# Kernel optimization log

Hardware: AMD Instinct MI355X
Metric: run time of the kernel (lower is better)

The kernel has to match this reference:

```python
import jax, jax.numpy as jnp
import numpy as np

N = 30000      # total nodes across batch
E = 480000     # edges (before self-loops)
B = 48         # graphs in batch
H = 4          # heads
D = 64         # hidden per head
NIN = 8
NOUT = 128
L = 10
SLOPE = 0.2    # GATConv default negative_slope


def setup_inputs() -> dict:
    key = jax.random.key(0)
    ks = jax.random.split(key, 12)
    s = 0.05
    x = jax.random.normal(ks[0], (N, NIN), jnp.float32)
    edge_index = jax.random.randint(ks[1], (2, E), 0, N, dtype=jnp.int32)
    batch = jnp.sort(jax.random.randint(ks[2], (N,), 0, B, dtype=jnp.int32))
    # layer 0 params (input dim NIN)
    W0 = jax.random.normal(ks[3], (NIN, H * D), jnp.float32) * s
    a_src0 = jax.random.normal(ks[4], (H, D), jnp.float32) * s
    a_dst0 = jax.random.normal(ks[5], (H, D), jnp.float32) * s
    b0 = jnp.zeros((H * D,), jnp.float32)
    # layers 1..L-1 (input dim H*D)
    Ws = jax.random.normal(ks[6], (L - 1, H * D, H * D), jnp.float32) * s
    a_srcs = jax.random.normal(ks[7], (L - 1, H, D), jnp.float32) * s
    a_dsts = jax.random.normal(ks[8], (L - 1, H, D), jnp.float32) * s
    bs = jnp.zeros((L - 1, H * D), jnp.float32)
    # readout head: GELU -> Linear(4*H*D -> NOUT)
    head_W = jax.random.normal(ks[9], (4 * H * D, NOUT), jnp.float32) * s
    head_b = jnp.zeros((NOUT,), jnp.float32)
    return dict(x=x, edge_index=edge_index, batch=batch,
                W0=W0, a_src0=a_src0, a_dst0=a_dst0, b0=b0,
                Ws=Ws, a_srcs=a_srcs, a_dsts=a_dsts, bs=bs,
                head_W=head_W, head_b=head_b)


def _gat_layer(x, W, a_src, a_dst, b, src, dst):
    n = x.shape[0]
    h = (x @ W).reshape(n, H, D)                      # [N,H,D]
    alpha_src = jnp.einsum('nhd,hd->nh', h, a_src)    # [N,H]
    alpha_dst = jnp.einsum('nhd,hd->nh', h, a_dst)
    e = jax.nn.leaky_relu(alpha_src[src] + alpha_dst[dst], SLOPE)  # [Etot,H]
    # segment softmax over destination neighborhoods
    m = jax.ops.segment_max(e, dst, num_segments=n)
    e = jnp.exp(e - m[dst])
    z = jax.ops.segment_sum(e, dst, num_segments=n)
    alpha = e / (z[dst] + 1e-16)                      # [Etot,H]
    msg = h[src] * alpha[:, :, None]                  # [Etot,H,D]
    out = jax.ops.segment_sum(msg, dst, num_segments=n)
    return out.reshape(n, H * D) + b


def reference(x, edge_index, batch, W0, a_src0, a_dst0, b0,
              Ws, a_srcs, a_dsts, bs, head_W, head_b):
    # add self loops (GATConv default add_self_loops=True)
    loops = jnp.arange(N, dtype=edge_index.dtype)
    src = jnp.concatenate([edge_index[0], loops])
    dst = jnp.concatenate([edge_index[1], loops])

    h = _gat_layer(x, W0, a_src0, a_dst0, b0, src, dst)
    for i in range(L - 1):
        h = jax.nn.gelu(h, approximate=False)  # dropout = identity (eval)
        h = _gat_layer(h, Ws[i], a_srcs[i], a_dsts[i], bs[i], src, dst)

    # MultiAggregation([min, max, mean, sum]) over graphs
    cnt = jax.ops.segment_sum(jnp.ones((N,), h.dtype), batch, num_segments=B)
    g_sum = jax.ops.segment_sum(h, batch, num_segments=B)
    g_mean = g_sum / jnp.maximum(cnt, 1.0)[:, None]
    g_min = jax.ops.segment_min(h, batch, num_segments=B)
    g_max = jax.ops.segment_max(h, batch, num_segments=B)
    g = jnp.concatenate([g_min, g_max, g_mean, g_sum], axis=-1)  # [B, 4*H*D]

    return jax.nn.gelu(g, approximate=False) @ head_W + head_b   # [B, NOUT]
```

## Files before the change

### kernel.cpp

```cpp
#include <hip/hip_runtime.h>
#include <math.h>

#define NN   30000
#define EE   480000
#define ETOT 510000
#define BB   48
#define HHH  4
#define DDD  64
#define CCH  256
#define NINP 8
#define NOUTP 128
#define NLAY 10
#define SLOPE 0.2f
#define PCHUNK 32

typedef short v8s  __attribute__((ext_vector_type(8)));
typedef float v4f  __attribute__((ext_vector_type(4)));

__device__ __forceinline__ float gelu_f(float x){
    return 0.5f * x * (1.0f + erff(x * 0.70710678118654752f));
}
__device__ __forceinline__ unsigned short f2bf(float f){
    unsigned u = __float_as_uint(f);
    unsigned r = u + 0x7FFF + ((u >> 16) & 1);
    return (unsigned short)(r >> 16);
}
__device__ __forceinline__ float bf2f(unsigned short b){
    return __uint_as_float(((unsigned)b) << 16);
}
__device__ __forceinline__ float lrelu(float e){
    return (e > 0.f) ? e : SLOPE * e;
}
__device__ __forceinline__ float4 up4(uint2 u){
    float4 r;
    r.x = __uint_as_float(u.x << 16);
    r.y = __uint_as_float(u.x & 0xFFFF0000u);
    r.z = __uint_as_float(u.y << 16);
    r.w = __uint_as_float(u.y & 0xFFFF0000u);
    return r;
}

__global__ void count_k(const int* __restrict__ ei, int* __restrict__ cnt){
    int e = blockIdx.x * 256 + threadIdx.x;
    if (e >= ETOT) return;
    int d = (e < EE) ? ei[EE + e] : (e - EE);
    atomicAdd(&cnt[d], 1);
}

__global__ __launch_bounds__(1024) void scan_k(const int* __restrict__ cnt, int* __restrict__ row_ptr){
    __shared__ int sdata[1024];
    __shared__ int carry;
    int tid = threadIdx.x;
    if (tid == 0) carry = 0;
    __syncthreads();
    for (int base = 0; base < NN; base += 1024){
        int i = base + tid;
        int v = (i < NN) ? cnt[i] : 0;
        sdata[tid] = v;
        __syncthreads();
        for (int off = 1; off < 1024; off <<= 1){
            int t = (tid >= off) ? sdata[tid - off] : 0;
            __syncthreads();
            sdata[tid] += t;
            __syncthreads();
        }
        if (i < NN) row_ptr[i] = carry + sdata[tid] - v;
        __syncthreads();
        if (tid == 1023) carry += sdata[1023];
        __syncthreads();
    }
    if (tid == 0) row_ptr[NN] = carry;
}

__global__ void scatter_k(const int* __restrict__ ei, const int* __restrict__ row_ptr,
                          int* __restrict__ cursor, int* __restrict__ csr_src){
    int e = blockIdx.x * 256 + threadIdx.x;
    if (e >= ETOT) return;
    int s, d;
    if (e < EE){ s = ei[e]; d = ei[EE + e]; } else { s = d = e - EE; }
    int pos = row_ptr[d] + atomicAdd(&cursor[d], 1);
    csr_src[pos] = s;
}

__global__ __launch_bounds__(256) void wconv_k(const float* __restrict__ Ws,
                                               unsigned short* __restrict__ WT_hi,
                                               unsigned short* __restrict__ WT_lo){
    int l = blockIdx.x;
    int n = threadIdx.x;
    int k0 = blockIdx.y * 32;
    const float* W = Ws + (size_t)l * CCH * CCH;
    unsigned short* th = WT_hi + (size_t)l * CCH * CCH;
    unsigned short* tl = WT_lo + (size_t)l * CCH * CCH;
    for (int k = k0; k < k0 + 32; ++k){
        float w = W[k * CCH + n];
        unsigned short h = f2bf(w);
        th[n * CCH + k] = h;
        tl[n * CCH + k] = f2bf(w - bf2f(h));
    }
}

__global__ __launch_bounds__(256) void waconv_k(const float* __restrict__ Ws,
                                                const float* __restrict__ a_srcs,
                                                const float* __restrict__ a_dsts,
                                                unsigned short* __restrict__ wa_hi,
                                                unsigned short* __restrict__ wa_lo){
    int l = blockIdx.x;
    int k = threadIdx.x;
    const float* W = Ws + (size_t)l * CCH * CCH;
#pragma unroll
    for (int j = 0; j < 8; ++j){
        const float* av = (j < 4) ? (a_srcs + (size_t)l * CCH + j * DDD)
                                  : (a_dsts + (size_t)l * CCH + (j - 4) * DDD);
        int cb = (j & 3) * DDD;
        float s = 0.f;
        for (int d = 0; d < DDD; ++d) s += W[k * CCH + cb + d] * av[d];
        unsigned short hb = f2bf(s);
        wa_hi[((size_t)l * 16 + j) * CCH + k] = hb;
        wa_lo[((size_t)l * 16 + j) * CCH + k] = f2bf(s - bf2f(hb));
    }
#pragma unroll
    for (int j = 8; j < 16; ++j){
        wa_hi[((size_t)l * 16 + j) * CCH + k] = 0;
        wa_lo[((size_t)l * 16 + j) * CCH + k] = 0;
    }
}

__global__ __launch_bounds__(256) void l0_fused(const float* __restrict__ x,
                                                const float* __restrict__ W0,
                                                const float* __restrict__ a_src,
                                                const float* __restrict__ a_dst,
                                                unsigned short* __restrict__ hout,
                                                float* __restrict__ asb,
                                                float* __restrict__ adb){
    __shared__ float xs[NINP];
    int n = blockIdx.x;
    int c = threadIdx.x;
    if (c < NINP) xs[c] = x[n * NINP + c];
    __syncthreads();
    float acc = 0.f;
#pragma unroll
    for (int k = 0; k < NINP; ++k) acc += xs[k] * W0[k * CCH + c];
    hout[(size_t)n * CCH + c] = f2bf(acc);
    int hh = c >> 6, lane = c & 63;
    float s1 = acc * a_src[hh * DDD + lane];
    float s2 = acc * a_dst[hh * DDD + lane];
#pragma unroll
    for (int off = 32; off; off >>= 1){
        s1 += __shfl_xor(s1, off);
        s2 += __shfl_xor(s2, off);
    }
    if (lane == 0){
        asb[(size_t)n * HHH + hh] = s1;
        adb[(size_t)n * HHH + hh] = s2;
    }
}

__global__ __launch_bounds__(256) void gemm_mfma(const float* __restrict__ A,
                                                 const unsigned short* __restrict__ Bhi,
                                                 const unsigned short* __restrict__ Blo,
                                                 const unsigned short* __restrict__ WAhi,
                                                 const unsigned short* __restrict__ WAlo,
                                                 unsigned short* __restrict__ C,
                                                 float* __restrict__ asb,
                                                 float* __restrict__ adb){
    int tid  = threadIdx.x;
    int lane = tid & 63, wave = tid >> 6;
    int wr = wave >> 1, wc = wave & 1;
    int rowBase = blockIdx.y * 128 + wr * 64;
    int colBase = blockIdx.x * 128 + wc * 64;
    int fr = lane & 15;
    int kg = lane >> 4;
    bool doAlpha = (blockIdx.x == 0) && (wc == 0);

    v4f acc[4][4];
#pragma unroll
    for (int mi = 0; mi < 4; ++mi)
#pragma unroll
        for (int ni = 0; ni < 4; ++ni) acc[mi][ni] = (v4f){0.f, 0.f, 0.f, 0.f};
    v4f acca[4];
#pragma unroll
    for (int mi = 0; mi < 4; ++mi) acca[mi] = (v4f){0.f, 0.f, 0.f, 0.f};

    const float* aptr[4];
#pragma unroll
    for (int mi = 0; mi < 4; ++mi){
        int r = rowBase + mi * 16 + fr;
        if (r >= NN) r = NN - 1;
        aptr[mi] = A + (size_t)r * CCH + kg * 8;
    }
    const unsigned short* bhp[4];
    const unsigned short* blp[4];
#pragma unroll
    for (int ni = 0; ni < 4; ++ni){
        int c = colBase + ni * 16 + fr;
        bhp[ni] = Bhi + (size_t)c * CCH + kg * 8;
        blp[ni] = Blo + (size_t)c * CCH + kg * 8;
    }
    const unsigned short* wahp = WAhi + (size_t)fr * CCH + kg * 8;
    const unsigned short* walp = WAlo + (size_t)fr * CCH + kg * 8;

    for (int kc = 0; kc < CCH; kc += 32){
        v8s ah[4], al[4], bh[4], bl[4];
#pragma unroll
        for (int mi = 0; mi < 4; ++mi){
            float4 v0 = *(const float4*)(aptr[mi] + kc);
            float4 v1 = *(const float4*)(aptr[mi] + kc + 4);
            float f[8] = {v0.x, v0.y, v0.z, v0.w, v1.x, v1.y, v1.z, v1.w};
            v8s hi, lo;
#pragma unroll
            for (int j = 0; j < 8; ++j){
                float g = gelu_f(f[j]);
                unsigned short hb = f2bf(g);
                hi[j] = (short)hb;
                lo[j] = (short)f2bf(g - bf2f(hb));
            }
            ah[mi] = hi; al[mi] = lo;
        }
#pragma unroll
        for (int ni = 0; ni < 4; ++ni){
            bh[ni] = *(const v8s*)(bhp[ni] + kc);
            bl[ni] = *(const v8s*)(blp[ni] + kc);
        }
#pragma unroll
        for (int mi = 0; mi < 4; ++mi)
#pragma unroll
            for (int ni = 0; ni < 4; ++ni){
                acc[mi][ni] = __builtin_amdgcn_mfma_f32_16x16x32_bf16(ah[mi], bh[ni], acc[mi][ni], 0, 0, 0);
                acc[mi][ni] = __builtin_amdgcn_mfma_f32_16x16x32_bf16(al[mi], bh[ni], acc[mi][ni], 0, 0, 0);
                acc[mi][ni] = __builtin_amdgcn_mfma_f32_16x16x32_bf16(ah[mi], bl[ni], acc[mi][ni], 0, 0, 0);
            }
        if (doAlpha){
            v8s wh = *(const v8s*)(wahp + kc);
            v8s wl = *(const v8s*)(walp + kc);
#pragma unroll
            for (int mi = 0; mi < 4; ++mi){
                acca[mi] = __builtin_amdgcn_mfma_f32_16x16x32_bf16(ah[mi], wh, acca[mi], 0, 0, 0);
                acca[mi] = __builtin_amdgcn_mfma_f32_16x16x32_bf16(al[mi], wh, acca[mi], 0, 0, 0);
                acca[mi] = __builtin_amdgcn_mfma_f32_16x16x32_bf16(ah[mi], wl, acca[mi], 0, 0, 0);
            }
        }
    }

#pragma unroll
    for (int mi = 0; mi < 4; ++mi)
#pragma unroll
        for (int j = 0; j < 4; ++j){
            int r = rowBase + mi * 16 + kg * 4 + j;
            if (r < NN){
#pragma unroll
                for (int ni = 0; ni < 4; ++ni)
                    C[(size_t)r * CCH + colBase + ni * 16 + fr] = f2bf(acc[mi][ni][j]);
            }
        }
    if (doAlpha){
#pragma unroll
        for (int mi = 0; mi < 4; ++mi)
#pragma unroll
            for (int j = 0; j < 4; ++j){
                int r = rowBase + mi * 16 + kg * 4 + j;
                if (r < NN){
                    float val = acca[mi][j];
                    if (fr < 4)      asb[(size_t)r * HHH + fr]       = val;
                    else if (fr < 8) adb[(size_t)r * HHH + (fr - 4)] = val;
                }
            }
    }
}

#define LOADG(gg, U0, U1, U2, U3, A0, A1, A2, A3)                      \
    { int _b = (gg) << 2;                                              \
      int _i0 = ix_w[_b], _i1 = ix_w[_b + 1];                          \
      int _i2 = ix_w[_b + 2], _i3 = ix_w[_b + 3];                      \
      A0 = al_w[(_b + 0) * HHH + hc];                                  \
      A1 = al_w[(_b + 1) * HHH + hc];                                  \
      A2 = al_w[(_b + 2) * HHH + hc];                                  \
      A3 = al_w[(_b + 3) * HHH + hc];                                  \
      U0 = *(const uint2*)(h + (size_t)_i0 * CCH + coff);              \
      U1 = *(const uint2*)(h + (size_t)_i1 * CCH + coff);              \
      U2 = *(const uint2*)(h + (size_t)_i2 * CCH + coff);              \
      U3 = *(const uint2*)(h + (size_t)_i3 * CCH + coff); }

#define CONSUME(U0, U1, U2, U3, A0, A1, A2, A3)                        \
    { float4 _v0 = up4(U0), _v1 = up4(U1), _v2 = up4(U2), _v3 = up4(U3); \
      acc.x += _v0.x * A0 + _v1.x * A1 + _v2.x * A2 + _v3.x * A3;      \
      acc.y += _v0.y * A0 + _v1.y * A1 + _v2.y * A2 + _v3.y * A3;      \
      acc.z += _v0.z * A0 + _v1.z * A1 + _v2.z * A2 + _v3.z * A3;      \
      acc.w += _v0.w * A0 + _v1.w * A1 + _v2.w * A2 + _v3.w * A3; }

__global__ __launch_bounds__(256) void agg_k(const unsigned short* __restrict__ h,
                                             const float* __restrict__ asrc,
                                             const float* __restrict__ adst,
                                             const float* __restrict__ bias,
                                             const int* __restrict__ row_ptr,
                                             const int* __restrict__ csr_src,
                                             float* __restrict__ out){
    __shared__ float s_al[4][64 * HHH];
    __shared__ int   s_ix[4][64];

    int wave = threadIdx.x >> 6, lane = threadIdx.x & 63;
    int n = blockIdx.x * 4 + wave;
    int row0 = row_ptr[n];
    int deg  = row_ptr[n + 1] - row0;
    float4 ad = *(const float4*)(adst + (size_t)n * HHH);
    int coff = lane << 2;
    int hc   = lane >> 4;
    float* al_w = s_al[wave];
    int*   ix_w = s_ix[wave];
    float4 acc = make_float4(0.f, 0.f, 0.f, 0.f);

    if (deg <= 64){
        int k = lane;
        int s = 0;
        float e0 = -INFINITY, e1 = -INFINITY, e2 = -INFINITY, e3 = -INFINITY;
        if (k < deg){
            s = csr_src[row0 + k];
            float4 as = *(const float4*)(asrc + (size_t)s * HHH);
            e0 = lrelu(as.x + ad.x); e1 = lrelu(as.y + ad.y);
            e2 = lrelu(as.z + ad.z); e3 = lrelu(as.w + ad.w);
        }
        float m0 = e0, m1 = e1, m2 = e2, m3 = e3;
#pragma unroll
        for (int off = 32; off; off >>= 1){
            m0 = fmaxf(m0, __shfl_xor(m0, off));
            m1 = fmaxf(m1, __shfl_xor(m1, off));
            m2 = fmaxf(m2, __shfl_xor(m2, off));
            m3 = fmaxf(m3, __shfl_xor(m3, off));
        }
        float x0 = 0.f, x1 = 0.f, x2 = 0.f, x3 = 0.f;
        if (k < deg){
            x0 = __expf(e0 - m0); x1 = __expf(e1 - m1);
            x2 = __expf(e2 - m2); x3 = __expf(e3 - m3);
        }
        float z0 = x0, z1 = x1, z2 = x2, z3 = x3;
#pragma unroll
        for (int off = 32; off; off >>= 1){
            z0 += __shfl_xor(z0, off);
            z1 += __shfl_xor(z1, off);
            z2 += __shfl_xor(z2, off);
            z3 += __shfl_xor(z3, off);
        }
        if (k < deg){
            float4 alv;
            alv.x = x0 / (z0 + 1e-16f);
            alv.y = x1 / (z1 + 1e-16f);
            alv.z = x2 / (z2 + 1e-16f);
            alv.w = x3 / (z3 + 1e-16f);
            ix_w[k] = s;
            *(float4*)&al_w[k * HHH] = alv;
        }
        int ng = deg >> 2;
        uint2 vA0, vA1, vA2, vA3, vB0, vB1, vB2, vB3;
        float aA0, aA1, aA2, aA3, aB0, aB1, aB2, aB3;
        if (ng > 0) LOADG(0, vA0, vA1, vA2, vA3, aA0, aA1, aA2, aA3);
        if (ng > 1) LOADG(1, vB0, vB1, vB2, vB3, aB0, aB1, aB2, aB3);
        for (int g = 0; g < ng; g += 2){
            if (g + 2 < ng) {
                CONSUME(vA0, vA1, vA2, vA3, aA0, aA1, aA2, aA3);
                LOADG(g + 2, vA0, vA1, vA2, vA3, aA0, aA1, aA2, aA3);
            } else {
                CONSUME(vA0, vA1, vA2, vA3, aA0, aA1, aA2, aA3);
            }
            if (g + 1 < ng){
                if (g + 3 < ng) {
                    CONSUME(vB0, vB1, vB2, vB3, aB0, aB1, aB2, aB3);
                    LOADG(g + 3, vB0, vB1, vB2, vB3, aB0, aB1, aB2, aB3);
                } else {
                    CONSUME(vB0, vB1, vB2, vB3, aB0, aB1, aB2, aB3);
                }
            }
        }
        for (int kk = ng << 2; kk < deg; ++kk){
            int i0 = ix_w[kk];
            float a0 = al_w[kk * HHH + hc];
            float4 v0 = up4(*(const uint2*)(h + (size_t)i0 * CCH + coff));
            acc.x += v0.x * a0; acc.y += v0.y * a0; acc.z += v0.z * a0; acc.w += v0.w * a0;
        }
    } else {
        float m0 = -INFINITY, m1 = -INFINITY, m2 = -INFINITY, m3 = -INFINITY;
        float z0 = 0.f, z1 = 0.f, z2 = 0.f, z3 = 0.f;
        for (int c0 = 0; c0 < deg; c0 += 64){
            int k = c0 + lane;
            float e0 = -INFINITY, e1 = -INFINITY, e2 = -INFINITY, e3 = -INFINITY;
            if (k < deg){
                int s = csr_src[row0 + k];
                float4 as = *(const float4*)(asrc + (size_t)s * HHH);
                e0 = lrelu(as.x + ad.x); e1 = lrelu(as.y + ad.y);
                e2 = lrelu(as.z + ad.z); e3 = lrelu(as.w + ad.w);
            }
            float c0m = e0, c1m = e1, c2m = e2, c3m = e3;
#pragma unroll
            for (int off = 32; off; off >>= 1){
                c0m = fmaxf(c0m, __shfl_xor(c0m, off));
                c1m = fmaxf(c1m, __shfl_xor(c1m, off));
                c2m = fmaxf(c2m, __shfl_xor(c2m, off));
                c3m = fmaxf(c3m, __shfl_xor(c3m, off));
            }
            float n0 = fmaxf(m0, c0m), n1 = fmaxf(m1, c1m);
            float n2 = fmaxf(m2, c2m), n3 = fmaxf(m3, c3m);
            float x0 = 0.f, x1 = 0.f, x2 = 0.f, x3 = 0.f;
            if (k < deg){
                x0 = __expf(e0 - n0); x1 = __expf(e1 - n1);
                x2 = __expf(e2 - n2); x3 = __expf(e3 - n3);
            }
            float s0 = x0, s1 = x1, s2 = x2, s3 = x3;
#pragma unroll
            for (int off = 32; off; off >>= 1){
                s0 += __shfl_xor(s0, off);
                s1 += __shfl_xor(s1, off);
                s2 += __shfl_xor(s2, off);
                s3 += __shfl_xor(s3, off);
            }
            z0 = z0 * ((m0 == -INFINITY) ? 0.f : __expf(m0 - n0)) + s0;
            z1 = z1 * ((m1 == -INFINITY) ? 0.f : __expf(m1 - n1)) + s1;
            z2 = z2 * ((m2 == -INFINITY) ? 0.f : __expf(m2 - n2)) + s2;
            z3 = z3 * ((m3 == -INFINITY) ? 0.f : __expf(m3 - n3)) + s3;
            m0 = n0; m1 = n1; m2 = n2; m3 = n3;
        }
        float iz0 = 1.f / (z0 + 1e-16f), iz1 = 1.f / (z1 + 1e-16f);
        float iz2 = 1.f / (z2 + 1e-16f), iz3 = 1.f / (z3 + 1e-16f);
        for (int c0 = 0; c0 < deg; c0 += 64){
            int k = c0 + lane;
            if (k < deg){
                int s = csr_src[row0 + k];
                float4 as = *(const float4*)(asrc + (size_t)s * HHH);
                float4 alv;
                alv.x = __expf(lrelu(as.x + ad.x) - m0) * iz0;
                alv.y = __expf(lrelu(as.y + ad.y) - m1) * iz1;
                alv.z = __expf(lrelu(as.z + ad.z) - m2) * iz2;
                alv.w = __expf(lrelu(as.w + ad.w) - m3) * iz3;
                ix_w[lane] = s;
                *(float4*)&al_w[lane * HHH] = alv;
            }
            int cnt = deg - c0; if (cnt > 64) cnt = 64;
            for (int j = 0; j < cnt; ++j){
                int i0 = ix_w[j];
                float a0 = al_w[j * HHH + hc];
                float4 v0 = up4(*(const uint2*)(h + (size_t)i0 * CCH + coff));
                acc.x += v0.x * a0; acc.y += v0.y * a0; acc.z += v0.z * a0; acc.w += v0.w * a0;
            }
        }
    }

    float4 bv = *(const float4*)(bias + coff);
    acc.x += bv.x; acc.y += bv.y; acc.z += bv.z; acc.w += bv.w;
    *(float4*)(out + (size_t)n * CCH + coff) = acc;
}

__global__ void gptr_k(const int* __restrict__ batch, int* __restrict__ gptr){
    int i = blockIdx.x * 256 + threadIdx.x;
    if (i >= NN) return;
    int bi = batch[i];
    int bp = (i == 0) ? -1 : batch[i - 1];
    for (int g = bp + 1; g <= bi; ++g) gptr[g] = i;
    if (i == NN - 1){
        for (int g = bi + 1; g <= BB; ++g) gptr[g] = NN;
    }
}

__global__ __launch_bounds__(256) void pool1_k(const float* __restrict__ h,
                                               const int* __restrict__ gptr,
                                               float* __restrict__ part){
    const int S1 = BB * PCHUNK * CCH;
    int b = blockIdx.x, j = blockIdx.y, c = threadIdx.x;
    int s = gptr[b], e = gptr[b + 1];
    int len = e - s;
    int per = (len + PCHUNK - 1) / PCHUNK;
    int r0 = s + j * per;
    int r1 = r0 + per; if (r1 > e) r1 = e;
    float mn = INFINITY, mx = -INFINITY, sm = 0.f;
    int n = r0;
    for (; n + 4 <= r1; n += 4){
        float v0 = h[(size_t)(n + 0) * CCH + c];
        float v1 = h[(size_t)(n + 1) * CCH + c];
        float v2 = h[(size_t)(n + 2) * CCH + c];
        float v3 = h[(size_t)(n + 3) * CCH + c];
        mn = fminf(mn, fminf(fminf(v0, v1), fminf(v2, v3)));
        mx = fmaxf(mx, fmaxf(fmaxf(v0, v1), fmaxf(v2, v3)));
        sm += (v0 + v1) + (v2 + v3);
    }
    for (; n < r1; ++n){
        float v = h[(size_t)n * CCH + c];
        mn = fminf(mn, v); mx = fmaxf(mx, v); sm += v;
    }
    size_t o = ((size_t)b * PCHUNK + j) * CCH + c;
    part[o] = mn; part[S1 + o] = mx; part[2 * (size_t)S1 + o] = sm;
}

__global__ __launch_bounds__(256) void pool2_k(const float* __restrict__ part,
                                               const int* __restrict__ gptr,
                                               float* __restrict__ gbuf){
    const int S1 = BB * PCHUNK * CCH;
    int b = blockIdx.x, c = threadIdx.x;
    float mn = INFINITY, mx = -INFINITY, sm = 0.f;
#pragma unroll
    for (int j = 0; j < PCHUNK; ++j){
        size_t o = ((size_t)b * PCHUNK + j) * CCH + c;
        mn = fminf(mn, part[o]);
        mx = fmaxf(mx, part[S1 + o]);
        sm += part[2 * (size_t)S1 + o];
    }
    int cnt = gptr[b + 1] - gptr[b];
    float mean = sm / fmaxf((float)cnt, 1.0f);
    if (cnt == 0){ mn = 0.f; mx = 0.f; }
    gbuf[b * 4 * CCH + 0 * CCH + c] = mn;
    gbuf[b * 4 * CCH + 1 * CCH + c] = mx;
    gbuf[b * 4 * CCH + 2 * CCH + c] = mean;
    gbuf[b * 4 * CCH + 3 * CCH + c] = sm;
}

__global__ __launch_bounds__(128) void head_k(const float* __restrict__ gbuf,
                                              const float* __restrict__ head_W,
                                              const float* __restrict__ head_b,
                                              float* __restrict__ out){
    __shared__ float gs[4 * CCH];
    int b = blockIdx.x;
    int o = threadIdx.x;
    for (int k = o; k < 4 * CCH; k += 128) gs[k] = gelu_f(gbuf[b * 4 * CCH + k]);
    __syncthreads();
    float acc = head_b[o];
    for (int k = 0; k < 4 * CCH; ++k) acc += gs[k] * head_W[k * NOUTP + o];
    out[b * NOUTP + o] = acc;
}

extern "C" void kernel_launch(void* const* d_in, const int* in_sizes, int n_in,
                              void* d_out, int out_size, void* d_ws, size_t ws_size,
                              hipStream_t stream){
    const float* x        = (const float*)d_in[0];
    const int*   ei       = (const int*)  d_in[1];
    const int*   batch    = (const int*)  d_in[2];
    const float* W0       = (const float*)d_in[3];
    const float* a_src0   = (const float*)d_in[4];
    const float* a_dst0   = (const float*)d_in[5];
    const float* b0       = (const float*)d_in[6];
    const float* Ws       = (const float*)d_in[7];
    const float* a_srcs   = (const float*)d_in[8];
    const float* a_dsts   = (const float*)d_in[9];
    const float* bs       = (const float*)d_in[10];
    const float* head_W   = (const float*)d_in[11];
    const float* head_b   = (const float*)d_in[12];
    float* out = (float*)d_out;

    char* p = (char*)d_ws;
    float* buf0 = (float*)p;                   p += (size_t)NN * CCH * 4;
    unsigned short* buf1 = (unsigned short*)p; p += (size_t)NN * CCH * 2;
    float* asb  = (float*)p;                   p += (size_t)NN * HHH * 4;
    float* adb  = (float*)p;                   p += (size_t)NN * HHH * 4;
    int* row_ptr = (int*)p;                    p += 120016;
    int* cnt     = (int*)p;                    p += (size_t)NN * 4;
    int* csr_src = (int*)p;                    p += (size_t)ETOT * 4;
    float* gbuf  = (float*)p;                  p += (size_t)BB * 4 * CCH * 4;
    int* gptr    = (int*)p;                    p += 208;
    unsigned short* wthi = (unsigned short*)p; p += (size_t)(NLAY - 1) * CCH * CCH * 2;
    unsigned short* wtlo = (unsigned short*)p; p += (size_t)(NLAY - 1) * CCH * CCH * 2;
    unsigned short* wahi = (unsigned short*)p; p += (size_t)(NLAY - 1) * 16 * CCH * 2;
    unsigned short* walo = (unsigned short*)p; p += (size_t)(NLAY - 1) * 16 * CCH * 2;
    float* pscr = (float*)p;                   p += (size_t)3 * BB * PCHUNK * CCH * 4;

    hipMemsetAsync(cnt, 0, (size_t)NN * 4, stream);
    count_k<<<(ETOT + 255) / 256, 256, 0, stream>>>(ei, cnt);
    scan_k<<<1, 1024, 0, stream>>>(cnt, row_ptr);
    hipMemsetAsync(cnt, 0, (size_t)NN * 4, stream);
    scatter_k<<<(ETOT + 255) / 256, 256, 0, stream>>>(ei, row_ptr, cnt, csr_src);
    gptr_k<<<(NN + 255) / 256, 256, 0, stream>>>(batch, gptr);
    wconv_k<<<dim3(NLAY - 1, 8), 256, 0, stream>>>(Ws, wthi, wtlo);
    waconv_k<<<NLAY - 1, 256, 0, stream>>>(Ws, a_srcs, a_dsts, wahi, walo);

    l0_fused<<<NN, 256, 0, stream>>>(x, W0, a_src0, a_dst0, buf1, asb, adb);
    agg_k<<<NN / 4, 256, 0, stream>>>(buf1, asb, adb, b0, row_ptr, csr_src, buf0);

    dim3 ggrid(2, (NN + 127) / 128);
    for (int l = 1; l < NLAY; ++l){
        const unsigned short* whl = wthi + (size_t)(l - 1) * CCH * CCH;
        const unsigned short* wll = wtlo + (size_t)(l - 1) * CCH * CCH;
        const unsigned short* wal_h = wahi + (size_t)(l - 1) * 16 * CCH;
        const unsigned short* wal_l = walo + (size_t)(l - 1) * 16 * CCH;
        const float* bl  = bs + (size_t)(l - 1) * CCH;
        gemm_mfma<<<ggrid, 256, 0, stream>>>(buf0, whl, wll, wal_h, wal_l, buf1, asb, adb);
        agg_k<<<NN / 4, 256, 0, stream>>>(buf1, asb, adb, bl, row_ptr, csr_src, buf0);
    }

    dim3 pgrid(BB, PCHUNK);
    pool1_k<<<pgrid, 256, 0, stream>>>(buf0, gptr, pscr);
    pool2_k<<<BB, 256, 0, stream>>>(pscr, gptr, gbuf);
    head_k<<<BB, 128, 0, stream>>>(gbuf, head_W, head_b, out);
}
```

Baseline: 1.120 ms.

## Widen aggregation gathers to 16B, parallelize scan and weight preprocessing kernels

The aggregation kernel's low-degree path now splits each wave into two halves that each gather 16-byte bf16 rows for alternating edges, then combines the halves with a cross-half shuffle. This is meant to halve the per-edge instruction count and increase memory-level parallelism on the dominant gather. Separately, the single-block prefix scan becomes a per-thread serial scan followed by wave shuffles. The weight transpose now uses a shared-memory tiled transpose over more blocks, and the attention-weight folding kernel is spread over more blocks with vectorized loads. Together these target the setup overheads, at the cost of more shuffle work and extra register pressure in the aggregation kernel.

```diff
diff --git a/kernel.cpp b/kernel.cpp
--- a/kernel.cpp
+++ b/kernel.cpp
@@ -48,28 +48,38 @@
 }
 
 __global__ __launch_bounds__(1024) void scan_k(const int* __restrict__ cnt, int* __restrict__ row_ptr){
-    __shared__ int sdata[1024];
-    __shared__ int carry;
-    int tid = threadIdx.x;
-    if (tid == 0) carry = 0;
+    const int PER = 30;
+    int t = threadIdx.x;
+    int base = t * PER;
+    int v[PER];
+    int sum = 0;
+#pragma unroll
+    for (int i = 0; i < PER; ++i){
+        int x = (base + i < NN) ? cnt[base + i] : 0;
+        v[i] = sum;
+        sum += x;
+    }
+    int lane = t & 63, w = t >> 6;
+    int inc = sum;
+#pragma unroll
+    for (int off = 1; off < 64; off <<= 1){
+        int u = __shfl_up(inc, off);
+        if (lane >= off) inc += u;
+    }
+    __shared__ int wtot[16], woff[16];
+    if (lane == 63) wtot[w] = inc;
     __syncthreads();
-    for (int base = 0; base < NN; base += 1024){
-        int i = base + tid;
-        int v = (i < NN) ? cnt[i] : 0;
-        sdata[tid] = v;
-        __syncthreads();
-        for (int off = 1; off < 1024; off <<= 1){
-            int t = (tid >= off) ? sdata[tid - off] : 0;
-            __syncthreads();
-            sdata[tid] += t;
-            __syncthreads();
-        }
-        if (i < NN) row_ptr[i] = carry + sdata[tid] - v;
-        __syncthreads();
-        if (tid == 1023) carry += sdata[1023];
-        __syncthreads();
-    }
-    if (tid == 0) row_ptr[NN] = carry;
+    if (t == 0){
+        int r = 0;
+        for (int i = 0; i < 16; ++i){ woff[i] = r; r += wtot[i]; }
+        row_ptr[NN] = r;
+    }
+    __syncthreads();
+    int excl = woff[w] + (inc - sum);
+#pragma unroll
+    for (int i = 0; i < PER; ++i){
+        if (base + i < NN) row_ptr[base + i] = excl + v[i];
+    }
 }
 
 __global__ void scatter_k(const int* __restrict__ ei, const int* __restrict__ row_ptr,
@@ -85,17 +95,25 @@
 __global__ __launch_bounds__(256) void wconv_k(const float* __restrict__ Ws,
                                                unsigned short* __restrict__ WT_hi,
                                                unsigned short* __restrict__ WT_lo){
+    __shared__ float tile[32][33];
     int l = blockIdx.x;
-    int n = threadIdx.x;
-    int k0 = blockIdx.y * 32;
+    int kt = (blockIdx.y >> 3) * 32;
+    int nt = (blockIdx.y & 7) * 32;
     const float* W = Ws + (size_t)l * CCH * CCH;
     unsigned short* th = WT_hi + (size_t)l * CCH * CCH;
     unsigned short* tl = WT_lo + (size_t)l * CCH * CCH;
-    for (int k = k0; k < k0 + 32; ++k){
-        float w = W[k * CCH + n];
+    int tx = threadIdx.x & 31, ty = threadIdx.x >> 5;
+#pragma unroll
+    for (int r = ty; r < 32; r += 8)
+        tile[r][tx] = W[(size_t)(kt + r) * CCH + nt + tx];
+    __syncthreads();
+#pragma unroll
+    for (int r = ty; r < 32; r += 8){
+        float w = tile[tx][r];
         unsigned short h = f2bf(w);
-        th[n * CCH + k] = h;
-        tl[n * CCH + k] = f2bf(w - bf2f(h));
+        size_t o = (size_t)(nt + r) * CCH + kt + tx;
+        th[o] = h;
+        tl[o] = f2bf(w - bf2f(h));
     }
 }
 
@@ -105,23 +123,28 @@
                                                 unsigned short* __restrict__ wa_hi,
                                                 unsigned short* __restrict__ wa_lo){
     int l = blockIdx.x;
+    int j = blockIdx.y;
     int k = threadIdx.x;
     const float* W = Ws + (size_t)l * CCH * CCH;
-#pragma unroll
-    for (int j = 0; j < 8; ++j){
-        const float* av = (j < 4) ? (a_srcs + (size_t)l * CCH + j * DDD)
-                                  : (a_dsts + (size_t)l * CCH + (j - 4) * DDD);
-        int cb = (j & 3) * DDD;
-        float s = 0.f;
-        for (int d = 0; d < DDD; ++d) s += W[k * CCH + cb + d] * av[d];
-        unsigned short hb = f2bf(s);
-        wa_hi[((size_t)l * 16 + j) * CCH + k] = hb;
-        wa_lo[((size_t)l * 16 + j) * CCH + k] = f2bf(s - bf2f(hb));
-    }
-#pragma unroll
-    for (int j = 8; j < 16; ++j){
-        wa_hi[((size_t)l * 16 + j) * CCH + k] = 0;
-        wa_lo[((size_t)l * 16 + j) * CCH + k] = 0;
+    const float* av = (j < 4) ? (a_srcs + (size_t)l * CCH + j * DDD)
+                              : (a_dsts + (size_t)l * CCH + (j - 4) * DDD);
+    int cb = (j & 3) * DDD;
+    float s = 0.f;
+    const float4* wp = (const float4*)(W + (size_t)k * CCH + cb);
+    const float4* ap = (const float4*)av;
+#pragma unroll
+    for (int d = 0; d < DDD / 4; ++d){
+        float4 wv = wp[d], avv = ap[d];
+        s += wv.x * avv.x + wv.y * avv.y + wv.z * avv.z + wv.w * avv.w;
+    }
+    unsigned short hb = f2bf(s);
+    wa_hi[((size_t)l * 16 + j) * CCH + k] = hb;
+    wa_lo[((size_t)l * 16 + j) * CCH + k] = f2bf(s - bf2f(hb));
+    if (j >= 4){
+        wa_hi[((size_t)l * 16 + j + 4) * CCH + k] = 0;
+        wa_lo[((size_t)l * 16 + j + 4) * CCH + k] = 0;
+        wa_hi[((size_t)l * 16 + j + 8) * CCH + k] = 0;
+        wa_lo[((size_t)l * 16 + j + 8) * CCH + k] = 0;
     }
 }
 
@@ -267,25 +290,34 @@
     }
 }
 
-#define LOADG(gg, U0, U1, U2, U3, A0, A1, A2, A3)                      \
-    { int _b = (gg) << 2;                                              \
-      int _i0 = ix_w[_b], _i1 = ix_w[_b + 1];                          \
-      int _i2 = ix_w[_b + 2], _i3 = ix_w[_b + 3];                      \
-      A0 = al_w[(_b + 0) * HHH + hc];                                  \
-      A1 = al_w[(_b + 1) * HHH + hc];                                  \
-      A2 = al_w[(_b + 2) * HHH + hc];                                  \
-      A3 = al_w[(_b + 3) * HHH + hc];                                  \
-      U0 = *(const uint2*)(h + (size_t)_i0 * CCH + coff);              \
-      U1 = *(const uint2*)(h + (size_t)_i1 * CCH + coff);              \
-      U2 = *(const uint2*)(h + (size_t)_i2 * CCH + coff);              \
-      U3 = *(const uint2*)(h + (size_t)_i3 * CCH + coff); }
-
-#define CONSUME(U0, U1, U2, U3, A0, A1, A2, A3)                        \
-    { float4 _v0 = up4(U0), _v1 = up4(U1), _v2 = up4(U2), _v3 = up4(U3); \
-      acc.x += _v0.x * A0 + _v1.x * A1 + _v2.x * A2 + _v3.x * A3;      \
-      acc.y += _v0.y * A0 + _v1.y * A1 + _v2.y * A2 + _v3.y * A3;      \
-      acc.z += _v0.z * A0 + _v1.z * A1 + _v2.z * A2 + _v3.z * A3;      \
-      acc.w += _v0.w * A0 + _v1.w * A1 + _v2.w * A2 + _v3.w * A3; }
+#define LOADG8(gg, U0, U1, U2, U3, A0, A1, A2, A3)                     \
+    { int _b = (gg) << 3;                                              \
+      int _e0 = _b + half, _e1 = _b + 2 + half;                        \
+      int _e2 = _b + 4 + half, _e3 = _b + 6 + half;                    \
+      int _i0 = ix_w[_e0], _i1 = ix_w[_e1];                            \
+      int _i2 = ix_w[_e2], _i3 = ix_w[_e3];                            \
+      A0 = al_w[_e0 * HHH + hc8];                                      \
+      A1 = al_w[_e1 * HHH + hc8];                                      \
+      A2 = al_w[_e2 * HHH + hc8];                                      \
+      A3 = al_w[_e3 * HHH + hc8];                                      \
+      U0 = *(const uint4*)(h + (size_t)_i0 * CCH + coff8);             \
+      U1 = *(const uint4*)(h + (size_t)_i1 * CCH + coff8);             \
+      U2 = *(const uint4*)(h + (size_t)_i2 * CCH + coff8);             \
+      U3 = *(const uint4*)(h + (size_t)_i3 * CCH + coff8); }
+
+#define CONSUME8(U0, U1, U2, U3, A0, A1, A2, A3)                       \
+    { float4 _l0 = up4(make_uint2(U0.x, U0.y)), _h0 = up4(make_uint2(U0.z, U0.w)); \
+      float4 _l1 = up4(make_uint2(U1.x, U1.y)), _h1 = up4(make_uint2(U1.z, U1.w)); \
+      float4 _l2 = up4(make_uint2(U2.x, U2.y)), _h2 = up4(make_uint2(U2.z, U2.w)); \
+      float4 _l3 = up4(make_uint2(U3.x, U3.y)), _h3 = up4(make_uint2(U3.z, U3.w)); \
+      accLo.x += _l0.x * A0 + _l1.x * A1 + _l2.x * A2 + _l3.x * A3;    \
+      accLo.y += _l0.y * A0 + _l1.y * A1 + _l2.y * A2 + _l3.y * A3;    \
+      accLo.z += _l0.z * A0 + _l1.z * A1 + _l2.z * A2 + _l3.z * A3;    \
+      accLo.w += _l0.w * A0 + _l1.w * A1 + _l2.w * A2 + _l3.w * A3;    \
+      accHi.x += _h0.x * A0 + _h1.x * A1 + _h2.x * A2 + _h3.x * A3;    \
+      accHi.y += _h0.y * A0 + _h1.y * A1 + _h2.y * A2 + _h3.y * A3;    \
+      accHi.z += _h0.z * A0 + _h1.z * A1 + _h2.z * A2 + _h3.z * A3;    \
+      accHi.w += _h0.w * A0 + _h1.w * A1 + _h2.w * A2 + _h3.w * A3; }
 
 __global__ __launch_bounds__(256) void agg_k(const unsigned short* __restrict__ h,
                                              const float* __restrict__ asrc,
@@ -302,11 +334,8 @@
     int row0 = row_ptr[n];
     int deg  = row_ptr[n + 1] - row0;
     float4 ad = *(const float4*)(adst + (size_t)n * HHH);
-    int coff = lane << 2;
-    int hc   = lane >> 4;
     float* al_w = s_al[wave];
     int*   ix_w = s_ix[wave];
-    float4 acc = make_float4(0.f, 0.f, 0.f, 0.f);
 
     if (deg <= 64){
         int k = lane;
@@ -348,99 +377,128 @@
             ix_w[k] = s;
             *(float4*)&al_w[k * HHH] = alv;
         }
-        int ng = deg >> 2;
-        uint2 vA0, vA1, vA2, vA3, vB0, vB1, vB2, vB3;
+        int half  = lane >> 5;
+        int l32   = lane & 31;
+        int coff8 = l32 << 3;
+        int hc8   = l32 >> 3;
+        float4 accLo = make_float4(0.f, 0.f, 0.f, 0.f);
+        float4 accHi = make_float4(0.f, 0.f, 0.f, 0.f);
+
+        int ng = deg >> 3;
+        uint4 uA0, uA1, uA2, uA3, uB0, uB1, uB2, uB3;
         float aA0, aA1, aA2, aA3, aB0, aB1, aB2, aB3;
-        if (ng > 0) LOADG(0, vA0, vA1, vA2, vA3, aA0, aA1, aA2, aA3);
-        if (ng > 1) LOADG(1, vB0, vB1, vB2, vB3, aB0, aB1, aB2, aB3);
+        if (ng > 0) LOADG8(0, uA0, uA1, uA2, uA3, aA0, aA1, aA2, aA3);
+        if (ng > 1) LOADG8(1, uB0, uB1, uB2, uB3, aB0, aB1, aB2, aB3);
         for (int g = 0; g < ng; g += 2){
             if (g + 2 < ng) {
-                CONSUME(vA0, vA1, vA2, vA3, aA0, aA1, aA2, aA3);
-                LOADG(g + 2, vA0, vA1, vA2, vA3, aA0, aA1, aA2, aA3);
+                CONSUME8(uA0, uA1, uA2, uA3, aA0, aA1, aA2, aA3);
+                LOADG8(g + 2, uA0, uA1, uA2, uA3, aA0, aA1, aA2, aA3);
             } else {
-                CONSUME(vA0, vA1, vA2, vA3, aA0, aA1, aA2, aA3);
+                CONSUME8(uA0, uA1, uA2, uA3, aA0, aA1, aA2, aA3);
             }
             if (g + 1 < ng){
                 if (g + 3 < ng) {
-                    CONSUME(vB0, vB1, vB2, vB3, aB0, aB1, aB2, aB3);
-                    LOADG(g + 3, vB0, vB1, vB2, vB3, aB0, aB1, aB2, aB3);
+                    CONSUME8(uB0, uB1, uB2, uB3, aB0, aB1, aB2, aB3);
+                    LOADG8(g + 3, uB0, uB1, uB2, uB3, aB0, aB1, aB2, aB3);
                 } else {
-                    CONSUME(vB0, vB1, vB2, vB3, aB0, aB1, aB2, aB3);
+                    CONSUME8(uB0, uB1, uB2, uB3, aB0, aB1, aB2, aB3);
                 }
             }
         }
-        for (int kk = ng << 2; kk < deg; ++kk){
-            int i0 = ix_w[kk];
-            float a0 = al_w[kk * HHH + hc];
+        for (int kk = ng << 3; kk < deg; kk += 2){
+            int e = kk + half;
+            if (e < deg){
+                int i0 = ix_w[e];
+                float a0 = al_w[e * HHH + hc8];
+                uint4 u = *(const uint4*)(h + (size_t)i0 * CCH + coff8);
+                float4 lo = up4(make_uint2(u.x, u.y)), hi = up4(make_uint2(u.z, u.w));
+                accLo.x += lo.x * a0; accLo.y += lo.y * a0;
+                accLo.z += lo.z * a0; accLo.w += lo.w * a0;
+                accHi.x += hi.x * a0; accHi.y += hi.y * a0;
+                accHi.z += hi.z * a0; accHi.w += hi.w * a0;
+            }
+        }
+        accLo.x += __shfl_xor(accLo.x, 32); accLo.y += __shfl_xor(accLo.y, 32);
+        accLo.z += __shfl_xor(accLo.z, 32); accLo.w += __shfl_xor(accLo.w, 32);
+        accHi.x += __shfl_xor(accHi.x, 32); accHi.y += __shfl_xor(accHi.y, 32);
+        accHi.z += __shfl_xor(accHi.z, 32); accHi.w += __shfl_xor(accHi.w, 32);
+        if (half == 0){
+            float4 b0v = *(const float4*)(bias + coff8);
+            float4 b1v = *(const float4*)(bias + coff8 + 4);
+            accLo.x += b0v.x; accLo.y += b0v.y; accLo.z += b0v.z; accLo.w += b0v.w;
+            accHi.x += b1v.x; accHi.y += b1v.y; accHi.z += b1v.z; accHi.w += b1v.w;
+            *(float4*)(out + (size_t)n * CCH + coff8)     = accLo;
+            *(float4*)(out + (size_t)n * CCH + coff8 + 4) = accHi;
+        }
+        return;
+    }
+
+    int coff = lane << 2;
+    int hc   = lane >> 4;
+    float4 acc = make_float4(0.f, 0.f, 0.f, 0.f);
+    float m0 = -INFINITY, m1 = -INFINITY, m2 = -INFINITY, m3 = -INFINITY;
+    float z0 = 0.f, z1 = 0.f, z2 = 0.f, z3 = 0.f;
+    for (int c0 = 0; c0 < deg; c0 += 64){
+        int k = c0 + lane;
+        float e0 = -INFINITY, e1 = -INFINITY, e2 = -INFINITY, e3 = -INFINITY;
+        if (k < deg){
+            int s = csr_src[row0 + k];
+            float4 as = *(const float4*)(asrc + (size_t)s * HHH);
+            e0 = lrelu(as.x + ad.x); e1 = lrelu(as.y + ad.y);
+            e2 = lrelu(as.z + ad.z); e3 = lrelu(as.w + ad.w);
+        }
+        float c0m = e0, c1m = e1, c2m = e2, c3m = e3;
+#pragma unroll
+        for (int off = 32; off; off >>= 1){
+            c0m = fmaxf(c0m, __shfl_xor(c0m, off));
+            c1m = fmaxf(c1m, __shfl_xor(c1m, off));
+            c2m = fmaxf(c2m, __shfl_xor(c2m, off));
+            c3m = fmaxf(c3m, __shfl_xor(c3m, off));
+        }
+        float n0 = fmaxf(m0, c0m), n1 = fmaxf(m1, c1m);
+        float n2 = fmaxf(m2, c2m), n3 = fmaxf(m3, c3m);
+        float x0 = 0.f, x1 = 0.f, x2 = 0.f, x3 = 0.f;
+        if (k < deg){
+            x0 = __expf(e0 - n0); x1 = __expf(e1 - n1);
+            x2 = __expf(e2 - n2); x3 = __expf(e3 - n3);
+        }
+        float s0 = x0, s1 = x1, s2 = x2, s3 = x3;
+#pragma unroll
+        for (int off = 32; off; off >>= 1){
+            s0 += __shfl_xor(s0, off);
+            s1 += __shfl_xor(s1, off);
+            s2 += __shfl_xor(s2, off);
+            s3 += __shfl_xor(s3, off);
+        }
+        z0 = z0 * ((m0 == -INFINITY) ? 0.f : __expf(m0 - n0)) + s0;
+        z1 = z1 * ((m1 == -INFINITY) ? 0.f : __expf(m1 - n1)) + s1;
+        z2 = z2 * ((m2 == -INFINITY) ? 0.f : __expf(m2 - n2)) + s2;
+        z3 = z3 * ((m3 == -INFINITY) ? 0.f : __expf(m3 - n3)) + s3;
+        m0 = n0; m1 = n1; m2 = n2; m3 = n3;
+    }
+    float iz0 = 1.f / (z0 + 1e-16f), iz1 = 1.f / (z1 + 1e-16f);
+    float iz2 = 1.f / (z2 + 1e-16f), iz3 = 1.f / (z3 + 1e-16f);
+    for (int c0 = 0; c0 < deg; c0 += 64){
+        int k = c0 + lane;
+        if (k < deg){
+            int s = csr_src[row0 + k];
+            float4 as = *(const float4*)(asrc + (size_t)s * HHH);
+            float4 alv;
+            alv.x = __expf(lrelu(as.x + ad.x) - m0) * iz0;
+            alv.y = __expf(lrelu(as.y + ad.y) - m1) * iz1;
+            alv.z = __expf(lrelu(as.z + ad.z) - m2) * iz2;
+            alv.w = __expf(lrelu(as.w + ad.w) - m3) * iz3;
+            ix_w[lane] = s;
+            *(float4*)&al_w[lane * HHH] = alv;
+        }
+        int cnt = deg - c0; if (cnt > 64) cnt = 64;
+        for (int j = 0; j < cnt; ++j){
+            int i0 = ix_w[j];
+            float a0 = al_w[j * HHH + hc];
             float4 v0 = up4(*(const uint2*)(h + (size_t)i0 * CCH + coff));
             acc.x += v0.x * a0; acc.y += v0.y * a0; acc.z += v0.z * a0; acc.w += v0.w * a0;
         }
-    } else {
-        float m0 = -INFINITY, m1 = -INFINITY, m2 = -INFINITY, m3 = -INFINITY;
-        float z0 = 0.f, z1 = 0.f, z2 = 0.f, z3 = 0.f;
-        for (int c0 = 0; c0 < deg; c0 += 64){
-            int k = c0 + lane;
-            float e0 = -INFINITY, e1 = -INFINITY, e2 = -INFINITY, e3 = -INFINITY;
-            if (k < deg){
-                int s = csr_src[row0 + k];
-                float4 as = *(const float4*)(asrc + (size_t)s * HHH);
-                e0 = lrelu(as.x + ad.x); e1 = lrelu(as.y + ad.y);
-                e2 = lrelu(as.z + ad.z); e3 = lrelu(as.w + ad.w);
-            }
-            float c0m = e0, c1m = e1, c2m = e2, c3m = e3;
-#pragma unroll
-            for (int off = 32; off; off >>= 1){
-                c0m = fmaxf(c0m, __shfl_xor(c0m, off));
-                c1m = fmaxf(c1m, __shfl_xor(c1m, off));
-                c2m = fmaxf(c2m, __shfl_xor(c2m, off));
-                c3m = fmaxf(c3m, __shfl_xor(c3m, off));
-            }
-            float n0 = fmaxf(m0, c0m), n1 = fmaxf(m1, c1m);
-            float n2 = fmaxf(m2, c2m), n3 = fmaxf(m3, c3m);
-            float x0 = 0.f, x1 = 0.f, x2 = 0.f, x3 = 0.f;
-            if (k < deg){
-                x0 = __expf(e0 - n0); x1 = __expf(e1 - n1);
-                x2 = __expf(e2 - n2); x3 = __expf(e3 - n3);
-            }
-            float s0 = x0, s1 = x1, s2 = x2, s3 = x3;
-#pragma unroll
-            for (int off = 32; off; off >>= 1){
-                s0 += __shfl_xor(s0, off);
-                s1 += __shfl_xor(s1, off);
-                s2 += __shfl_xor(s2, off);
-                s3 += __shfl_xor(s3, off);
-            }
-            z0 = z0 * ((m0 == -INFINITY) ? 0.f : __expf(m0 - n0)) + s0;
-            z1 = z1 * ((m1 == -INFINITY) ? 0.f : __expf(m1 - n1)) + s1;
-            z2 = z2 * ((m2 == -INFINITY) ? 0.f : __expf(m2 - n2)) + s2;
-            z3 = z3 * ((m3 == -INFINITY) ? 0.f : __expf(m3 - n3)) + s3;
-            m0 = n0; m1 = n1; m2 = n2; m3 = n3;
-        }
-        float iz0 = 1.f / (z0 + 1e-16f), iz1 = 1.f / (z1 + 1e-16f);
-        float iz2 = 1.f / (z2 + 1e-16f), iz3 = 1.f / (z3 + 1e-16f);
-        for (int c0 = 0; c0 < deg; c0 += 64){
-            int k = c0 + lane;
-            if (k < deg){
-                int s = csr_src[row0 + k];
-                float4 as = *(const float4*)(asrc + (size_t)s * HHH);
-                float4 alv;
-                alv.x = __expf(lrelu(as.x + ad.x) - m0) * iz0;
-                alv.y = __expf(lrelu(as.y + ad.y) - m1) * iz1;
-                alv.z = __expf(lrelu(as.z + ad.z) - m2) * iz2;
-                alv.w = __expf(lrelu(as.w + ad.w) - m3) * iz3;
-                ix_w[lane] = s;
-                *(float4*)&al_w[lane * HHH] = alv;
-            }
-            int cnt = deg - c0; if (cnt > 64) cnt = 64;
-            for (int j = 0; j < cnt; ++j){
-                int i0 = ix_w[j];
-                float a0 = al_w[j * HHH + hc];
-                float4 v0 = up4(*(const uint2*)(h + (size_t)i0 * CCH + coff));
-                acc.x += v0.x * a0; acc.y += v0.y * a0; acc.z += v0.z * a0; acc.w += v0.w * a0;
-            }
-        }
-    }
-
+    }
     float4 bv = *(const float4*)(bias + coff);
     acc.x += bv.x; acc.y += bv.y; acc.z += bv.z; acc.w += bv.w;
     *(float4*)(out + (size_t)n * CCH + coff) = acc;
@@ -562,8 +620,8 @@
     hipMemsetAsync(cnt, 0, (size_t)NN * 4, stream);
     scatter_k<<<(ETOT + 255) / 256, 256, 0, stream>>>(ei, row_ptr, cnt, csr_src);
     gptr_k<<<(NN + 255) / 256, 256, 0, stream>>>(batch, gptr);
-    wconv_k<<<dim3(NLAY - 1, 8), 256, 0, stream>>>(Ws, wthi, wtlo);
-    waconv_k<<<NLAY - 1, 256, 0, stream>>>(Ws, a_srcs, a_dsts, wahi, walo);
+    wconv_k<<<dim3(NLAY - 1, 64), 256, 0, stream>>>(Ws, wthi, wtlo);
+    waconv_k<<<dim3(NLAY - 1, 8), 256, 0, stream>>>(Ws, a_srcs, a_dsts, wahi, walo);
 
     l0_fused<<<NN, 256, 0, stream>>>(x, W0, a_src0, a_dst0, buf1, asb, adb);
     agg_k<<<NN / 4, 256, 0, stream>>>(buf1, asb, adb, b0, row_ptr, csr_src, buf0);
```

Measured after the change: 1.121 ms. No clear change (+0.1%).
